# Kernel optimization log

Measured on AMD Instinct MI355X. Metric: run time of the kernel, lower is better.

Reference implementation:

```python
import jax, jax.numpy as jnp
import numpy as np

STATE_DIM = 32
HIDDEN = 128
DT = 0.01


def _lstm_cell(inp, h, c, W, b):
    # inp: [B, D_in], h/c: [B, H], W: [D_in+H, 4H], b: [4H]
    gates = jnp.concatenate([inp, h], axis=-1) @ W + b
    i, f, g, o = jnp.split(gates, 4, axis=-1)
    i = jax.nn.sigmoid(i)
    f = jax.nn.sigmoid(f)
    g = jnp.tanh(g)
    o = jax.nn.sigmoid(o)
    c_new = f * c + i * g
    h_new = o * jnp.tanh(c_new)
    return h_new, c_new


def setup_inputs() -> dict:
    key = jax.random.key(0)
    ks = jax.random.split(key, 8)
    B = 8192
    s = lambda fan_in: 1.0 / np.sqrt(fan_in)
    W0 = jax.random.uniform(ks[0], (STATE_DIM + HIDDEN, 4 * HIDDEN), jnp.float32, -s(STATE_DIM + HIDDEN), s(STATE_DIM + HIDDEN))
    b0 = jax.random.uniform(ks[1], (4 * HIDDEN,), jnp.float32, -s(STATE_DIM + HIDDEN), s(STATE_DIM + HIDDEN))
    W1 = jax.random.uniform(ks[2], (HIDDEN + HIDDEN, 4 * HIDDEN), jnp.float32, -s(2 * HIDDEN), s(2 * HIDDEN))
    b1 = jax.random.uniform(ks[3], (4 * HIDDEN,), jnp.float32, -s(2 * HIDDEN), s(2 * HIDDEN))
    Wout = jax.random.uniform(ks[4], (HIDDEN, STATE_DIM), jnp.float32, -s(HIDDEN), s(HIDDEN))
    bout = jax.random.uniform(ks[5], (STATE_DIM,), jnp.float32, -s(HIDDEN), s(HIDDEN))
    dt_scale = jnp.ones((STATE_DIM,), jnp.float32) * 0.01
    x0 = jax.random.normal(ks[6], (B, STATE_DIM), jnp.float32)
    return {"x0": x0, "W0": W0, "b0": b0, "W1": W1, "b1": b1,
            "Wout": Wout, "bout": bout, "dt_scale": dt_scale, "num_steps": 512}


def reference(x0, W0, b0, W1, b1, Wout, bout, dt_scale, num_steps):
    B = x0.shape[0]
    h0 = jnp.zeros((B, HIDDEN), x0.dtype)
    c0 = jnp.zeros((B, HIDDEN), x0.dtype)

    def step(carry, _):
        x, h0_, c0_, h1_, c1_ = carry
        h0n, c0n = _lstm_cell(x, h0_, c0_, W0, b0)
        h1n, c1n = _lstm_cell(h0n, h1_, c1_, W1, b1)
        dx_dt = h1n @ Wout + bout
        x_new = x + dx_dt * dt_scale * DT
        return (x_new, h0n, c0n, h1n, c1n), x_new

    _, xs = jax.lax.scan(step, (x0, h0, c0, h0, c0), None, length=num_steps)
    # xs: [T, B, D] -> trajectory [B, T+1, D]
    traj = jnp.concatenate([x0[:, None, :], jnp.transpose(xs, (1, 0, 2))], axis=1)
    return traj
```

## Files before the change

### kernel.cpp

```cpp
#include <hip/hip_runtime.h>
#include <hip/hip_bf16.h>

typedef __bf16  bf16x8  __attribute__((ext_vector_type(8)));
typedef short   short8_t __attribute__((ext_vector_type(8)));
typedef float   float4_t __attribute__((ext_vector_type(4)));

#define MFMA(a, b, c) __builtin_amdgcn_mfma_f32_16x16x32_bf16((a), (b), (c), 0, 0, 0)

#define LOG2E      1.4426950408889634f
#define TWO_LOG2E  2.8853900817779268f

__device__ __forceinline__ unsigned short f2bf(float f) {
  unsigned u = __builtin_bit_cast(unsigned, f);
  unsigned r = ((u >> 16) & 1u) + 0x7FFFu;
  return (unsigned short)((u + r) >> 16);
}
__device__ __forceinline__ float sig2(float x) {
  return __builtin_amdgcn_rcpf(1.f + __builtin_amdgcn_exp2f(-x));
}
__device__ __forceinline__ float tanh2s(float x) {
  return 1.f - 2.f * __builtin_amdgcn_rcpf(1.f + __builtin_amdgcn_exp2f(x));
}

__global__ __launch_bounds__(512, 2) void lstm_roll(
    const float* __restrict__ x0,  const float* __restrict__ W0,
    const float* __restrict__ b0v, const float* __restrict__ W1,
    const float* __restrict__ b1v, const float* __restrict__ Wout,
    const float* __restrict__ bout, const float* __restrict__ dts,
    const int* __restrict__ nsp,   float* __restrict__ out)
{
  __shared__ __align__(16) unsigned short w0h[8 * 4 * 4 * 512];
  __shared__ __align__(16) unsigned short woutF[2 * 4 * 512];
  __shared__ __align__(16) unsigned short h0f[4 * 2 * 512];
  __shared__ __align__(16) unsigned short h1f[4 * 2 * 512];
  __shared__ __align__(16) unsigned short xf[2 * 512];

  const int tid = threadIdx.x;
  const int w   = tid >> 6;
  const int l   = tid & 63;
  const int lm  = l & 15;
  const int lh  = l >> 4;
  const int T   = nsp[0];
  const long rowStride = (long)(T + 1) * 32;
  const long bbase = (long)blockIdx.x * 32;

  bf16x8 w0x[4];
  bf16x8 w1f[4][8];
  #pragma unroll
  for (int g = 0; g < 4; ++g) {
    const float sc = (g == 2) ? TWO_LOG2E : LOG2E;
    const int col = g * 128 + w * 16 + lm;
    {
      short8_t t8;
      #pragma unroll
      for (int e = 0; e < 8; ++e) t8[e] = (short)f2bf(sc * W0[(lh * 8 + e) * 512 + col]);
      w0x[g] = __builtin_bit_cast(bf16x8, t8);
    }
    #pragma unroll
    for (int kt = 0; kt < 8; ++kt) {
      short8_t t8;
      #pragma unroll
      for (int e = 0; e < 8; ++e) t8[e] = (short)f2bf(sc * W1[(kt * 32 + lh * 8 + e) * 512 + col]);
      w1f[g][kt] = __builtin_bit_cast(bf16x8, t8);
    }
    #pragma unroll
    for (int kt = 0; kt < 4; ++kt) {
      const int base = (((w * 4 + g) * 4) + kt) * 512 + l * 8;
      #pragma unroll
      for (int e = 0; e < 8; ++e)
        w0h[base + e] = f2bf(sc * W0[(32 + kt * 32 + lh * 8 + e) * 512 + col]);
    }
  }
  {
    const int n = w & 1, kt = w >> 1;
    if (kt < 4) {
      const float csc = dts[n * 16 + lm] * 0.01f;
      const int base = (n * 4 + kt) * 512 + l * 8;
      #pragma unroll
      for (int e = 0; e < 8; ++e)
        woutF[base + e] = f2bf(csc * Wout[(kt * 32 + lh * 8 + e) * 32 + (n * 16 + lm)]);
    }
  }
  float b0r[4], b1r[4];
  #pragma unroll
  for (int g = 0; g < 4; ++g) {
    const float sc = (g == 2) ? TWO_LOG2E : LOG2E;
    b0r[g] = sc * b0v[g * 128 + w * 16 + lm];
    b1r[g] = sc * b1v[g * 128 + w * 16 + lm];
  }

  const int m_c = w & 1, n_c = (w >> 1) & 1;
  float boutr = 0.f, xr[4] = {0.f, 0.f, 0.f, 0.f};
  long obase0 = 0;
  int  xfbase = 0;
  if (w < 4) {
    boutr = bout[n_c * 16 + lm] * dts[n_c * 16 + lm] * 0.01f;
    const int kin = n_c * 16 + lm;
    xfbase = m_c * 512 + (lh * 4 + 16 * (kin >> 3)) * 8 + (kin & 7);
    obase0 = (bbase + m_c * 16 + lh * 4) * rowStride + (n_c * 16 + lm);
    #pragma unroll
    for (int r = 0; r < 4; ++r) {
      xr[r] = x0[(bbase + m_c * 16 + lh * 4 + r) * 32 + n_c * 16 + lm];
      out[obase0 + r * rowStride] = xr[r];
      xf[xfbase + r * 8] = f2bf(xr[r]);
    }
  }
  for (int i = tid; i < 4 * 2 * 512; i += 512) { h0f[i] = 0; h1f[i] = 0; }

  const int hwb = ((w >> 1) * 2) * 512 +
                  (lh * 4 + 16 * (2 * (w & 1) + ((lm >> 3) & 1))) * 8 + (lm & 7);

  float4_t c0[2], c1[2];
  #pragma unroll
  for (int m = 0; m < 2; ++m) {
    c0[m] = (float4_t){0.f, 0.f, 0.f, 0.f};
    c1[m] = (float4_t){0.f, 0.f, 0.f, 0.f};
  }

  __syncthreads();

  #pragma unroll 1
  for (int t = 0; t < T; ++t) {
    float4_t acc0[2][4];
    #pragma unroll
    for (int g = 0; g < 4; ++g) {
      acc0[0][g] = (float4_t){b0r[g], b0r[g], b0r[g], b0r[g]};
      acc0[1][g] = (float4_t){b0r[g], b0r[g], b0r[g], b0r[g]};
    }
    #pragma unroll
    for (int kt = 0; kt < 4; ++kt) {
      const bf16x8 a0 = *(const bf16x8*)&h0f[(kt * 2 + 0) * 512 + l * 8];
      const bf16x8 a1 = *(const bf16x8*)&h0f[(kt * 2 + 1) * 512 + l * 8];
      #pragma unroll
      for (int g = 0; g < 4; ++g) {
        const bf16x8 bw = *(const bf16x8*)&w0h[(((w * 4 + g) * 4) + kt) * 512 + l * 8];
        acc0[0][g] = MFMA(a0, bw, acc0[0][g]);
        acc0[1][g] = MFMA(a1, bw, acc0[1][g]);
      }
    }
    if (w < 4 && t > 0) {
      float4_t dacc = (float4_t){boutr, boutr, boutr, boutr};
      #pragma unroll
      for (int kt = 0; kt < 4; ++kt) {
        const bf16x8 a  = *(const bf16x8*)&h1f[(kt * 2 + m_c) * 512 + l * 8];
        const bf16x8 bw = *(const bf16x8*)&woutF[(n_c * 4 + kt) * 512 + l * 8];
        dacc = MFMA(a, bw, dacc);
      }
      #pragma unroll
      for (int r = 0; r < 4; ++r) {
        xr[r] += dacc[r];
        xf[xfbase + r * 8] = f2bf(xr[r]);
      }
    }
    __syncthreads();

    {
      const bf16x8 ax0 = *(const bf16x8*)&xf[l * 8];
      #pragma unroll
      for (int g = 0; g < 4; ++g) acc0[0][g] = MFMA(ax0, w0x[g], acc0[0][g]);
      const bf16x8 ax1 = *(const bf16x8*)&xf[512 + l * 8];
      #pragma unroll
      for (int r = 0; r < 4; ++r) {
        const float iv = sig2(acc0[0][0][r]);
        const float fv = sig2(acc0[0][1][r]);
        const float gv = tanh2s(acc0[0][2][r]);
        const float ov = sig2(acc0[0][3][r]);
        const float cc = fv * c0[0][r] + iv * gv;
        c0[0][r] = cc;
        h0f[hwb + r * 8] = f2bf(ov * tanh2s(cc * TWO_LOG2E));
      }
      #pragma unroll
      for (int g = 0; g < 4; ++g) acc0[1][g] = MFMA(ax1, w0x[g], acc0[1][g]);
      #pragma unroll
      for (int r = 0; r < 4; ++r) {
        const float iv = sig2(acc0[1][0][r]);
        const float fv = sig2(acc0[1][1][r]);
        const float gv = tanh2s(acc0[1][2][r]);
        const float ov = sig2(acc0[1][3][r]);
        const float cc = fv * c0[1][r] + iv * gv;
        c0[1][r] = cc;
        h0f[hwb + 512 + r * 8] = f2bf(ov * tanh2s(cc * TWO_LOG2E));
      }
    }
    __syncthreads();

    if (w < 4 && t > 0) {
      const long ob = obase0 + (long)t * 32;
      #pragma unroll
      for (int r = 0; r < 4; ++r) out[ob + r * rowStride] = xr[r];
    }
    float4_t acc1[2][4];
    #pragma unroll
    for (int g = 0; g < 4; ++g) {
      acc1[0][g] = (float4_t){b1r[g], b1r[g], b1r[g], b1r[g]};
      acc1[1][g] = (float4_t){b1r[g], b1r[g], b1r[g], b1r[g]};
    }
    #pragma unroll
    for (int kt = 0; kt < 4; ++kt) {
      const bf16x8 a = *(const bf16x8*)&h0f[(kt * 2 + 0) * 512 + l * 8];
      #pragma unroll
      for (int g = 0; g < 4; ++g) acc1[0][g] = MFMA(a, w1f[g][kt], acc1[0][g]);
    }
    #pragma unroll
    for (int kt = 0; kt < 4; ++kt) {
      const bf16x8 a = *(const bf16x8*)&h1f[(kt * 2 + 0) * 512 + l * 8];
      #pragma unroll
      for (int g = 0; g < 4; ++g) acc1[0][g] = MFMA(a, w1f[g][kt + 4], acc1[0][g]);
    }
    float h1n[2][4];
    #pragma unroll
    for (int r = 0; r < 4; ++r) {
      const float iv = sig2(acc1[0][0][r]);
      const float fv = sig2(acc1[0][1][r]);
      const float gv = tanh2s(acc1[0][2][r]);
      const float ov = sig2(acc1[0][3][r]);
      const float cc = fv * c1[0][r] + iv * gv;
      c1[0][r] = cc;
      h1n[0][r] = ov * tanh2s(cc * TWO_LOG2E);
    }
    #pragma unroll
    for (int kt = 0; kt < 4; ++kt) {
      const bf16x8 a = *(const bf16x8*)&h0f[(kt * 2 + 1) * 512 + l * 8];
      #pragma unroll
      for (int g = 0; g < 4; ++g) acc1[1][g] = MFMA(a, w1f[g][kt], acc1[1][g]);
    }
    #pragma unroll
    for (int kt = 0; kt < 4; ++kt) {
      const bf16x8 a = *(const bf16x8*)&h1f[(kt * 2 + 1) * 512 + l * 8];
      #pragma unroll
      for (int g = 0; g < 4; ++g) acc1[1][g] = MFMA(a, w1f[g][kt + 4], acc1[1][g]);
    }
    #pragma unroll
    for (int r = 0; r < 4; ++r) {
      const float iv = sig2(acc1[1][0][r]);
      const float fv = sig2(acc1[1][1][r]);
      const float gv = tanh2s(acc1[1][2][r]);
      const float ov = sig2(acc1[1][3][r]);
      const float cc = fv * c1[1][r] + iv * gv;
      c1[1][r] = cc;
      h1n[1][r] = ov * tanh2s(cc * TWO_LOG2E);
    }
    __syncthreads();
    #pragma unroll
    for (int m = 0; m < 2; ++m)
      #pragma unroll
      for (int r = 0; r < 4; ++r)
        h1f[hwb + m * 512 + r * 8] = f2bf(h1n[m][r]);
    __syncthreads();
  }

  if (w < 4) {
    float4_t dacc = (float4_t){boutr, boutr, boutr, boutr};
    #pragma unroll
    for (int kt = 0; kt < 4; ++kt) {
      const bf16x8 a  = *(const bf16x8*)&h1f[(kt * 2 + m_c) * 512 + l * 8];
      const bf16x8 bw = *(const bf16x8*)&woutF[(n_c * 4 + kt) * 512 + l * 8];
      dacc = MFMA(a, bw, dacc);
    }
    const long ob = obase0 + (long)T * 32;
    #pragma unroll
    for (int r = 0; r < 4; ++r) {
      xr[r] += dacc[r];
      out[ob + r * rowStride] = xr[r];
    }
  }
}

extern "C" void kernel_launch(void* const* d_in, const int* in_sizes, int n_in,
                              void* d_out, int out_size, void* d_ws, size_t ws_size,
                              hipStream_t stream) {
  (void)n_in; (void)out_size; (void)d_ws; (void)ws_size;
  const float* x0   = (const float*)d_in[0];
  const float* W0   = (const float*)d_in[1];
  const float* b0   = (const float*)d_in[2];
  const float* W1   = (const float*)d_in[3];
  const float* b1   = (const float*)d_in[4];
  const float* Wout = (const float*)d_in[5];
  const float* bout = (const float*)d_in[6];
  const float* dts  = (const float*)d_in[7];
  const int*   nsp  = (const int*)d_in[8];
  float* out = (float*)d_out;

  const int B    = in_sizes[0] / 32;
  const int grid = B / 32;
  lstm_roll<<<dim3(grid), dim3(512), 0, stream>>>(x0, W0, b0, W1, b1, Wout, bout, dts, nsp, out);
}
```

Baseline: 2.475 ms.

## Double-buffer h1 state in LDS and use lighter LDS-only barriers

The layer-1 hidden state now lives in a ping-pong pair of LDS buffers. Each step reads the previous h1 from one half and writes the new h1 straight into the other half, which removes the register staging and one of the four per-step barriers. The bf16 copy of x reuses the write half, which holds a stale h1 at that point, so the separate xf buffer goes away, and the trajectory store moves earlier in the step. __syncthreads is replaced by a barrier that waits only on LDS counters, so outstanding global stores no longer stall each barrier. The risk is correctness, which depends on the parity bookkeeping and on the aliasing of x into the h1 buffer staying valid.

```diff
diff --git a/kernel.cpp b/kernel.cpp
--- a/kernel.cpp
+++ b/kernel.cpp
@@ -9,6 +9,12 @@
 
 #define LOG2E      1.4426950408889634f
 #define TWO_LOG2E  2.8853900817779268f
+
+#define BAR() do {                                            \
+    asm volatile("s_waitcnt lgkmcnt(0)" ::: "memory");        \
+    __builtin_amdgcn_s_barrier();                             \
+    asm volatile("" ::: "memory");                            \
+  } while (0)
 
 __device__ __forceinline__ unsigned short f2bf(float f) {
   unsigned u = __builtin_bit_cast(unsigned, f);
@@ -32,8 +38,7 @@
   __shared__ __align__(16) unsigned short w0h[8 * 4 * 4 * 512];
   __shared__ __align__(16) unsigned short woutF[2 * 4 * 512];
   __shared__ __align__(16) unsigned short h0f[4 * 2 * 512];
-  __shared__ __align__(16) unsigned short h1f[4 * 2 * 512];
-  __shared__ __align__(16) unsigned short xf[2 * 512];
+  __shared__ __align__(16) unsigned short h1f[2 * 4 * 2 * 512];
 
   const int tid = threadIdx.x;
   const int w   = tid >> 6;
@@ -102,7 +107,7 @@
     for (int r = 0; r < 4; ++r) {
       xr[r] = x0[(bbase + m_c * 16 + lh * 4 + r) * 32 + n_c * 16 + lm];
       out[obase0 + r * rowStride] = xr[r];
-      xf[xfbase + r * 8] = f2bf(xr[r]);
+      h1f[4096 + xfbase + r * 8] = f2bf(xr[r]);
     }
   }
   for (int i = tid; i < 4 * 2 * 512; i += 512) { h0f[i] = 0; h1f[i] = 0; }
@@ -117,10 +122,13 @@
     c1[m] = (float4_t){0.f, 0.f, 0.f, 0.f};
   }
 
-  __syncthreads();
+  BAR();
 
   #pragma unroll 1
   for (int t = 0; t < T; ++t) {
+    const int rpo = (t & 1) * 4096;
+    const int wpo = 4096 - rpo;
+
     float4_t acc0[2][4];
     #pragma unroll
     for (int g = 0; g < 4; ++g) {
@@ -142,23 +150,25 @@
       float4_t dacc = (float4_t){boutr, boutr, boutr, boutr};
       #pragma unroll
       for (int kt = 0; kt < 4; ++kt) {
-        const bf16x8 a  = *(const bf16x8*)&h1f[(kt * 2 + m_c) * 512 + l * 8];
+        const bf16x8 a  = *(const bf16x8*)&h1f[rpo + (kt * 2 + m_c) * 512 + l * 8];
         const bf16x8 bw = *(const bf16x8*)&woutF[(n_c * 4 + kt) * 512 + l * 8];
         dacc = MFMA(a, bw, dacc);
       }
+      const long ob = obase0 + (long)t * 32;
       #pragma unroll
       for (int r = 0; r < 4; ++r) {
         xr[r] += dacc[r];
-        xf[xfbase + r * 8] = f2bf(xr[r]);
-      }
-    }
-    __syncthreads();
+        h1f[wpo + xfbase + r * 8] = f2bf(xr[r]);
+        out[ob + r * rowStride] = xr[r];
+      }
+    }
+    BAR();
 
     {
-      const bf16x8 ax0 = *(const bf16x8*)&xf[l * 8];
+      const bf16x8 ax0 = *(const bf16x8*)&h1f[wpo + l * 8];
       #pragma unroll
       for (int g = 0; g < 4; ++g) acc0[0][g] = MFMA(ax0, w0x[g], acc0[0][g]);
-      const bf16x8 ax1 = *(const bf16x8*)&xf[512 + l * 8];
+      const bf16x8 ax1 = *(const bf16x8*)&h1f[wpo + 512 + l * 8];
       #pragma unroll
       for (int r = 0; r < 4; ++r) {
         const float iv = sig2(acc0[0][0][r]);
@@ -182,13 +192,8 @@
         h0f[hwb + 512 + r * 8] = f2bf(ov * tanh2s(cc * TWO_LOG2E));
       }
     }
-    __syncthreads();
-
-    if (w < 4 && t > 0) {
-      const long ob = obase0 + (long)t * 32;
-      #pragma unroll
-      for (int r = 0; r < 4; ++r) out[ob + r * rowStride] = xr[r];
-    }
+    BAR();
+
     float4_t acc1[2][4];
     #pragma unroll
     for (int g = 0; g < 4; ++g) {
@@ -203,11 +208,10 @@
     }
     #pragma unroll
     for (int kt = 0; kt < 4; ++kt) {
-      const bf16x8 a = *(const bf16x8*)&h1f[(kt * 2 + 0) * 512 + l * 8];
+      const bf16x8 a = *(const bf16x8*)&h1f[rpo + (kt * 2 + 0) * 512 + l * 8];
       #pragma unroll
       for (int g = 0; g < 4; ++g) acc1[0][g] = MFMA(a, w1f[g][kt + 4], acc1[0][g]);
     }
-    float h1n[2][4];
     #pragma unroll
     for (int r = 0; r < 4; ++r) {
       const float iv = sig2(acc1[0][0][r]);
@@ -216,7 +220,7 @@
       const float ov = sig2(acc1[0][3][r]);
       const float cc = fv * c1[0][r] + iv * gv;
       c1[0][r] = cc;
-      h1n[0][r] = ov * tanh2s(cc * TWO_LOG2E);
+      h1f[wpo + hwb + r * 8] = f2bf(ov * tanh2s(cc * TWO_LOG2E));
     }
     #pragma unroll
     for (int kt = 0; kt < 4; ++kt) {
@@ -226,7 +230,7 @@
     }
     #pragma unroll
     for (int kt = 0; kt < 4; ++kt) {
-      const bf16x8 a = *(const bf16x8*)&h1f[(kt * 2 + 1) * 512 + l * 8];
+      const bf16x8 a = *(const bf16x8*)&h1f[rpo + (kt * 2 + 1) * 512 + l * 8];
       #pragma unroll
       for (int g = 0; g < 4; ++g) acc1[1][g] = MFMA(a, w1f[g][kt + 4], acc1[1][g]);
     }
@@ -238,22 +242,17 @@
       const float ov = sig2(acc1[1][3][r]);
       const float cc = fv * c1[1][r] + iv * gv;
       c1[1][r] = cc;
-      h1n[1][r] = ov * tanh2s(cc * TWO_LOG2E);
-    }
-    __syncthreads();
-    #pragma unroll
-    for (int m = 0; m < 2; ++m)
-      #pragma unroll
-      for (int r = 0; r < 4; ++r)
-        h1f[hwb + m * 512 + r * 8] = f2bf(h1n[m][r]);
-    __syncthreads();
+      h1f[wpo + hwb + 512 + r * 8] = f2bf(ov * tanh2s(cc * TWO_LOG2E));
+    }
+    BAR();
   }
 
   if (w < 4) {
+    const int fin = (T & 1) * 4096;
     float4_t dacc = (float4_t){boutr, boutr, boutr, boutr};
     #pragma unroll
     for (int kt = 0; kt < 4; ++kt) {
-      const bf16x8 a  = *(const bf16x8*)&h1f[(kt * 2 + m_c) * 512 + l * 8];
+      const bf16x8 a  = *(const bf16x8*)&h1f[fin + (kt * 2 + m_c) * 512 + l * 8];
       const bf16x8 bw = *(const bf16x8*)&woutF[(n_c * 4 + kt) * 512 + l * 8];
       dacc = MFMA(a, bw, dacc);
     }
```

Measured after the change: 2.822 ms. +14.0%, slower.

## Skew two 16-row sub-batches across LSTM stages to overlap work between barriers

Applied to the files above, without the earlier changes.

Splits the 32-row block batch into two independent 16-row streams with separate shared buffers for h0, h1 and x. The streams are staggered so one stream's layer-1 cell and projection run alongside the other stream's layer-0 work inside each barrier interval. The output projection is split across warps per stream. The intent is to shorten the serial dependency chain per step and hide MFMA and transcendental latency behind independent work. In exchange the scheduling and indexing get more complex, register pressure may rise, and the number of barriers per step stays at four.

```diff
diff --git a/kernel.cpp b/kernel.cpp
--- a/kernel.cpp
+++ b/kernel.cpp
@@ -31,9 +31,12 @@
 {
   __shared__ __align__(16) unsigned short w0h[8 * 4 * 4 * 512];
   __shared__ __align__(16) unsigned short woutF[2 * 4 * 512];
-  __shared__ __align__(16) unsigned short h0f[4 * 2 * 512];
-  __shared__ __align__(16) unsigned short h1f[4 * 2 * 512];
-  __shared__ __align__(16) unsigned short xf[2 * 512];
+  __shared__ __align__(16) unsigned short h0f0[4 * 512];
+  __shared__ __align__(16) unsigned short h0f1[4 * 512];
+  __shared__ __align__(16) unsigned short h1f0[4 * 512];
+  __shared__ __align__(16) unsigned short h1f1[4 * 512];
+  __shared__ __align__(16) unsigned short xf0[512];
+  __shared__ __align__(16) unsigned short xf1[512];
 
   const int tid = threadIdx.x;
   const int w   = tid >> 6;
@@ -89,171 +92,178 @@
     b1r[g] = sc * b1v[g * 128 + w * 16 + lm];
   }
 
-  const int m_c = w & 1, n_c = (w >> 1) & 1;
+  const int S_w = (w >> 1) & 1;
+  const int n_c = w & 1;
   float boutr = 0.f, xr[4] = {0.f, 0.f, 0.f, 0.f};
   long obase0 = 0;
-  int  xfbase = 0;
+  int  xfb = 0;
   if (w < 4) {
     boutr = bout[n_c * 16 + lm] * dts[n_c * 16 + lm] * 0.01f;
     const int kin = n_c * 16 + lm;
-    xfbase = m_c * 512 + (lh * 4 + 16 * (kin >> 3)) * 8 + (kin & 7);
-    obase0 = (bbase + m_c * 16 + lh * 4) * rowStride + (n_c * 16 + lm);
+    xfb = (lh * 4 + 16 * (kin >> 3)) * 8 + (kin & 7);
+    obase0 = (bbase + S_w * 16 + lh * 4) * rowStride + (n_c * 16 + lm);
+    unsigned short* xfS = S_w ? xf1 : xf0;
     #pragma unroll
     for (int r = 0; r < 4; ++r) {
-      xr[r] = x0[(bbase + m_c * 16 + lh * 4 + r) * 32 + n_c * 16 + lm];
+      xr[r] = x0[(bbase + S_w * 16 + lh * 4 + r) * 32 + n_c * 16 + lm];
       out[obase0 + r * rowStride] = xr[r];
-      xf[xfbase + r * 8] = f2bf(xr[r]);
-    }
-  }
-  for (int i = tid; i < 4 * 2 * 512; i += 512) { h0f[i] = 0; h1f[i] = 0; }
-
-  const int hwb = ((w >> 1) * 2) * 512 +
+      xfS[xfb + r * 8] = f2bf(xr[r]);
+    }
+  }
+  for (int i = tid; i < 4 * 512; i += 512) {
+    h0f0[i] = 0; h0f1[i] = 0; h1f0[i] = 0; h1f1[i] = 0;
+  }
+
+  const int hwb = (w >> 1) * 512 +
                   (lh * 4 + 16 * (2 * (w & 1) + ((lm >> 3) & 1))) * 8 + (lm & 7);
 
-  float4_t c0[2], c1[2];
-  #pragma unroll
-  for (int m = 0; m < 2; ++m) {
-    c0[m] = (float4_t){0.f, 0.f, 0.f, 0.f};
-    c1[m] = (float4_t){0.f, 0.f, 0.f, 0.f};
+  float4_t c0s0 = {0.f,0.f,0.f,0.f}, c0s1 = {0.f,0.f,0.f,0.f};
+  float4_t c1s0 = {0.f,0.f,0.f,0.f}, c1s1 = {0.f,0.f,0.f,0.f};
+  float h1n1[4] = {0.f,0.f,0.f,0.f};
+
+#define INIT4(ACC, B) \
+    _Pragma("unroll") \
+    for (int g = 0; g < 4; ++g) (ACC)[g] = (float4_t){(B)[g], (B)[g], (B)[g], (B)[g]};
+
+#define CELL0H(HSRC, ACC) \
+    _Pragma("unroll") \
+    for (int kt = 0; kt < 4; ++kt) { \
+      const bf16x8 a = *(const bf16x8*)&(HSRC)[kt * 512 + l * 8]; \
+      _Pragma("unroll") \
+      for (int g = 0; g < 4; ++g) { \
+        const bf16x8 bw = *(const bf16x8*)&w0h[(((w * 4 + g) * 4) + kt) * 512 + l * 8]; \
+        (ACC)[g] = MFMA(a, bw, (ACC)[g]); \
+      } \
+    }
+
+#define XPART(XSRC, ACC) { \
+    const bf16x8 ax = *(const bf16x8*)&(XSRC)[l * 8]; \
+    _Pragma("unroll") \
+    for (int g = 0; g < 4; ++g) (ACC)[g] = MFMA(ax, w0x[g], (ACC)[g]); \
+  }
+
+#define CELL1A(H0SRC, AM) \
+    _Pragma("unroll") \
+    for (int kt = 0; kt < 4; ++kt) { \
+      const bf16x8 a = *(const bf16x8*)&(H0SRC)[kt * 512 + l * 8]; \
+      _Pragma("unroll") \
+      for (int g = 0; g < 4; ++g) (AM)[g] = MFMA(a, w1f[g][kt], (AM)[g]); \
+    }
+#define CELL1B(H1SRC, AM) \
+    _Pragma("unroll") \
+    for (int kt = 0; kt < 4; ++kt) { \
+      const bf16x8 a = *(const bf16x8*)&(H1SRC)[kt * 512 + l * 8]; \
+      _Pragma("unroll") \
+      for (int g = 0; g < 4; ++g) (AM)[g] = MFMA(a, w1f[g][kt + 4], (AM)[g]); \
+    }
+
+#define ACT4(ACC, CS, DST) \
+    _Pragma("unroll") \
+    for (int r = 0; r < 4; ++r) { \
+      const float iv = sig2((ACC)[0][r]); \
+      const float fv = sig2((ACC)[1][r]); \
+      const float gv = tanh2s((ACC)[2][r]); \
+      const float ov = sig2((ACC)[3][r]); \
+      const float cc = fv * (CS)[r] + iv * gv; \
+      (CS)[r] = cc; \
+      const float hv = ov * tanh2s(cc * TWO_LOG2E); \
+      DST; \
+    }
+
+#define PROJ(H1SRC, XFDST) { \
+    float4_t dacc = (float4_t){boutr, boutr, boutr, boutr}; \
+    _Pragma("unroll") \
+    for (int kt = 0; kt < 4; ++kt) { \
+      const bf16x8 a  = *(const bf16x8*)&(H1SRC)[kt * 512 + l * 8]; \
+      const bf16x8 bw = *(const bf16x8*)&woutF[(n_c * 4 + kt) * 512 + l * 8]; \
+      dacc = MFMA(a, bw, dacc); \
+    } \
+    _Pragma("unroll") \
+    for (int r = 0; r < 4; ++r) { \
+      xr[r] += dacc[r]; \
+      (XFDST)[xfb + r * 8] = f2bf(xr[r]); \
+    } \
   }
 
   __syncthreads();
 
   #pragma unroll 1
   for (int t = 0; t < T; ++t) {
-    float4_t acc0[2][4];
-    #pragma unroll
-    for (int g = 0; g < 4; ++g) {
-      acc0[0][g] = (float4_t){b0r[g], b0r[g], b0r[g], b0r[g]};
-      acc0[1][g] = (float4_t){b0r[g], b0r[g], b0r[g], b0r[g]};
-    }
+    float4_t acc0s0[4];
+    INIT4(acc0s0, b0r);
+    CELL0H(h0f0, acc0s0);
+    if (t > 0) {
+      #pragma unroll
+      for (int r = 0; r < 4; ++r) h1f1[hwb + r * 8] = f2bf(h1n1[r]);
+      if (w < 2) PROJ(h1f0, xf0);
+    }
+    __syncthreads();
+
+    float4_t acc0s1[4];
+    XPART(xf0, acc0s0);
+    INIT4(acc0s1, b0r);
+    CELL0H(h0f1, acc0s1);
+    ACT4(acc0s0, c0s0, h0f0[hwb + r * 8] = f2bf(hv));
+    if (w >= 2 && w < 4 && t > 0) PROJ(h1f1, xf1);
+    __syncthreads();
+
+    if (w < 2 && t > 0) {
+      const long ob = obase0 + (long)t * 32;
+      #pragma unroll
+      for (int r = 0; r < 4; ++r) out[ob + r * rowStride] = xr[r];
+    }
+    float h1n0[4];
+    {
+      float4_t am[4];
+      INIT4(am, b1r);
+      CELL1A(h0f0, am);
+      XPART(xf1, acc0s1);
+      ACT4(acc0s1, c0s1, h0f1[hwb + r * 8] = f2bf(hv));
+      CELL1B(h1f0, am);
+      ACT4(am, c1s0, h1n0[r] = hv);
+    }
+    __syncthreads();
+
+    if (w >= 2 && w < 4 && t > 0) {
+      const long ob = obase0 + (long)t * 32;
+      #pragma unroll
+      for (int r = 0; r < 4; ++r) out[ob + r * rowStride] = xr[r];
+    }
+    #pragma unroll
+    for (int r = 0; r < 4; ++r) h1f0[hwb + r * 8] = f2bf(h1n0[r]);
+    {
+      float4_t am[4];
+      INIT4(am, b1r);
+      CELL1A(h0f1, am);
+      CELL1B(h1f1, am);
+      ACT4(am, c1s1, h1n1[r] = hv);
+    }
+    __syncthreads();
+  }
+
+  #pragma unroll
+  for (int r = 0; r < 4; ++r) h1f1[hwb + r * 8] = f2bf(h1n1[r]);
+  if (w < 2) {
+    float4_t dacc = (float4_t){boutr, boutr, boutr, boutr};
     #pragma unroll
     for (int kt = 0; kt < 4; ++kt) {
-      const bf16x8 a0 = *(const bf16x8*)&h0f[(kt * 2 + 0) * 512 + l * 8];
-      const bf16x8 a1 = *(const bf16x8*)&h0f[(kt * 2 + 1) * 512 + l * 8];
-      #pragma unroll
-      for (int g = 0; g < 4; ++g) {
-        const bf16x8 bw = *(const bf16x8*)&w0h[(((w * 4 + g) * 4) + kt) * 512 + l * 8];
-        acc0[0][g] = MFMA(a0, bw, acc0[0][g]);
-        acc0[1][g] = MFMA(a1, bw, acc0[1][g]);
-      }
-    }
-    if (w < 4 && t > 0) {
-      float4_t dacc = (float4_t){boutr, boutr, boutr, boutr};
-      #pragma unroll
-      for (int kt = 0; kt < 4; ++kt) {
-        const bf16x8 a  = *(const bf16x8*)&h1f[(kt * 2 + m_c) * 512 + l * 8];
-        const bf16x8 bw = *(const bf16x8*)&woutF[(n_c * 4 + kt) * 512 + l * 8];
-        dacc = MFMA(a, bw, dacc);
-      }
-      #pragma unroll
-      for (int r = 0; r < 4; ++r) {
-        xr[r] += dacc[r];
-        xf[xfbase + r * 8] = f2bf(xr[r]);
-      }
-    }
-    __syncthreads();
-
-    {
-      const bf16x8 ax0 = *(const bf16x8*)&xf[l * 8];
-      #pragma unroll
-      for (int g = 0; g < 4; ++g) acc0[0][g] = MFMA(ax0, w0x[g], acc0[0][g]);
-      const bf16x8 ax1 = *(const bf16x8*)&xf[512 + l * 8];
-      #pragma unroll
-      for (int r = 0; r < 4; ++r) {
-        const float iv = sig2(acc0[0][0][r]);
-        const float fv = sig2(acc0[0][1][r]);
-        const float gv = tanh2s(acc0[0][2][r]);
-        const float ov = sig2(acc0[0][3][r]);
-        const float cc = fv * c0[0][r] + iv * gv;
-        c0[0][r] = cc;
-        h0f[hwb + r * 8] = f2bf(ov * tanh2s(cc * TWO_LOG2E));
-      }
-      #pragma unroll
-      for (int g = 0; g < 4; ++g) acc0[1][g] = MFMA(ax1, w0x[g], acc0[1][g]);
-      #pragma unroll
-      for (int r = 0; r < 4; ++r) {
-        const float iv = sig2(acc0[1][0][r]);
-        const float fv = sig2(acc0[1][1][r]);
-        const float gv = tanh2s(acc0[1][2][r]);
-        const float ov = sig2(acc0[1][3][r]);
-        const float cc = fv * c0[1][r] + iv * gv;
-        c0[1][r] = cc;
-        h0f[hwb + 512 + r * 8] = f2bf(ov * tanh2s(cc * TWO_LOG2E));
-      }
-    }
-    __syncthreads();
-
-    if (w < 4 && t > 0) {
-      const long ob = obase0 + (long)t * 32;
-      #pragma unroll
-      for (int r = 0; r < 4; ++r) out[ob + r * rowStride] = xr[r];
-    }
-    float4_t acc1[2][4];
-    #pragma unroll
-    for (int g = 0; g < 4; ++g) {
-      acc1[0][g] = (float4_t){b1r[g], b1r[g], b1r[g], b1r[g]};
-      acc1[1][g] = (float4_t){b1r[g], b1r[g], b1r[g], b1r[g]};
-    }
+      const bf16x8 a  = *(const bf16x8*)&h1f0[kt * 512 + l * 8];
+      const bf16x8 bw = *(const bf16x8*)&woutF[(n_c * 4 + kt) * 512 + l * 8];
+      dacc = MFMA(a, bw, dacc);
+    }
+    const long ob = obase0 + (long)T * 32;
+    #pragma unroll
+    for (int r = 0; r < 4; ++r) {
+      xr[r] += dacc[r];
+      out[ob + r * rowStride] = xr[r];
+    }
+  }
+  __syncthreads();
+  if (w >= 2 && w < 4) {
+    float4_t dacc = (float4_t){boutr, boutr, boutr, boutr};
     #pragma unroll
     for (int kt = 0; kt < 4; ++kt) {
-      const bf16x8 a = *(const bf16x8*)&h0f[(kt * 2 + 0) * 512 + l * 8];
-      #pragma unroll
-      for (int g = 0; g < 4; ++g) acc1[0][g] = MFMA(a, w1f[g][kt], acc1[0][g]);
-    }
-    #pragma unroll
-    for (int kt = 0; kt < 4; ++kt) {
-      const bf16x8 a = *(const bf16x8*)&h1f[(kt * 2 + 0) * 512 + l * 8];
-      #pragma unroll
-      for (int g = 0; g < 4; ++g) acc1[0][g] = MFMA(a, w1f[g][kt + 4], acc1[0][g]);
-    }
-    float h1n[2][4];
-    #pragma unroll
-    for (int r = 0; r < 4; ++r) {
-      const float iv = sig2(acc1[0][0][r]);
-      const float fv = sig2(acc1[0][1][r]);
-      const float gv = tanh2s(acc1[0][2][r]);
-      const float ov = sig2(acc1[0][3][r]);
-      const float cc = fv * c1[0][r] + iv * gv;
-      c1[0][r] = cc;
-      h1n[0][r] = ov * tanh2s(cc * TWO_LOG2E);
-    }
-    #pragma unroll
-    for (int kt = 0; kt < 4; ++kt) {
-      const bf16x8 a = *(const bf16x8*)&h0f[(kt * 2 + 1) * 512 + l * 8];
-      #pragma unroll
-      for (int g = 0; g < 4; ++g) acc1[1][g] = MFMA(a, w1f[g][kt], acc1[1][g]);
-    }
-    #pragma unroll
-    for (int kt = 0; kt < 4; ++kt) {
-      const bf16x8 a = *(const bf16x8*)&h1f[(kt * 2 + 1) * 512 + l * 8];
-      #pragma unroll
-      for (int g = 0; g < 4; ++g) acc1[1][g] = MFMA(a, w1f[g][kt + 4], acc1[1][g]);
-    }
-    #pragma unroll
-    for (int r = 0; r < 4; ++r) {
-      const float iv = sig2(acc1[1][0][r]);
-      const float fv = sig2(acc1[1][1][r]);
-      const float gv = tanh2s(acc1[1][2][r]);
-      const float ov = sig2(acc1[1][3][r]);
-      const float cc = fv * c1[1][r] + iv * gv;
-      c1[1][r] = cc;
-      h1n[1][r] = ov * tanh2s(cc * TWO_LOG2E);
-    }
-    __syncthreads();
-    #pragma unroll
-    for (int m = 0; m < 2; ++m)
-      #pragma unroll
-      for (int r = 0; r < 4; ++r)
-        h1f[hwb + m * 512 + r * 8] = f2bf(h1n[m][r]);
-    __syncthreads();
-  }
-
-  if (w < 4) {
-    float4_t dacc = (float4_t){boutr, boutr, boutr, boutr};
-    #pragma unroll
-    for (int kt = 0; kt < 4; ++kt) {
-      const bf16x8 a  = *(const bf16x8*)&h1f[(kt * 2 + m_c) * 512 + l * 8];
+      const bf16x8 a  = *(const bf16x8*)&h1f1[kt * 512 + l * 8];
       const bf16x8 bw = *(const bf16x8*)&woutF[(n_c * 4 + kt) * 512 + l * 8];
       dacc = MFMA(a, bw, dacc);
     }
```

Measured after the change: 2.311 ms. -6.6%, faster.
